# Optimization experiments

Measured on AMD Instinct MI355X. Metric: run time of the kernel, lower is better.

## Reference

```python
import jax, jax.numpy as jnp
import numpy as np

# Mamba-2 dims (from wrapper: d_model=hidden_size=2048, d_state=64, d_conv=4, expand=2, headdim=64)
D_MODEL = 2048
EXPAND = 2
HEADDIM = 64
D_STATE = 64
D_CONV = 4
D_INNER = EXPAND * D_MODEL            # 4096
NHEADS = D_INNER // HEADDIM           # 64
NGROUPS = 1                           # mamba_ssm default
CONV_DIM = D_INNER + 2 * NGROUPS * D_STATE          # 4224
D_IN_PROJ = 2 * D_INNER + 2 * NGROUPS * D_STATE + NHEADS  # 8384
BATCH = 1
SEQLEN = 1024
RMS_EPS = 1e-5


def setup_inputs() -> dict:
    key = jax.random.key(0)
    ks = jax.random.split(key, 8)
    x = jax.random.normal(ks[0], (BATCH, SEQLEN, D_MODEL), jnp.float32)
    W_in = jax.random.normal(ks[1], (D_IN_PROJ, D_MODEL), jnp.float32) * 0.02
    conv_w = jax.random.normal(ks[2], (CONV_DIM, D_CONV), jnp.float32) * 0.2
    conv_b = jnp.zeros((CONV_DIM,), jnp.float32)
    # dt_bias so that softplus(dt_raw + dt_bias) lands in a realistic dt range ~[1e-3, 5e-2]
    dt_bias = jax.random.uniform(ks[3], (NHEADS,), jnp.float32, -6.0, -3.0)
    # A = -exp(A_log), A_log init like mamba_ssm: A ~ Uniform(1, 16)
    A_log = jnp.log(1.0 + 15.0 * jax.random.uniform(ks[4], (NHEADS,), jnp.float32))
    D = jnp.ones((NHEADS,), jnp.float32)
    norm_w = jnp.ones((D_INNER,), jnp.float32)
    W_out = jax.random.normal(ks[5], (D_MODEL, D_INNER), jnp.float32) * 0.02
    return {"x": x, "W_in": W_in, "conv_w": conv_w, "conv_b": conv_b,
            "dt_bias": dt_bias, "A_log": A_log, "D": D, "norm_w": norm_w, "W_out": W_out}


def reference(x, W_in, conv_w, conv_b, dt_bias, A_log, D, norm_w, W_out):
    B, T, _ = x.shape
    # input projection -> [z | xBC | dt]
    zxbcdt = jnp.einsum('btd,pd->btp', x, W_in)
    z = zxbcdt[..., :D_INNER]                                  # [B,T,D_INNER] gate
    xBC = zxbcdt[..., D_INNER:D_INNER + CONV_DIM]              # [B,T,CONV_DIM]
    dt = jax.nn.softplus(zxbcdt[..., D_INNER + CONV_DIM:] + dt_bias)  # [B,T,H]
    # causal depthwise conv1d (kernel D_CONV) + SiLU
    xp = jnp.pad(xBC, ((0, 0), (D_CONV - 1, 0), (0, 0)))
    conv = conv_b + sum(xp[:, k:k + T, :] * conv_w[:, k] for k in range(D_CONV))
    xBC = jax.nn.silu(conv)
    xh = xBC[..., :D_INNER].reshape(B, T, NHEADS, HEADDIM)     # [B,T,H,P]
    Bm = xBC[..., D_INNER:D_INNER + D_STATE]                   # [B,T,N] (ngroups=1)
    Cm = xBC[..., D_INNER + D_STATE:]                          # [B,T,N]
    A = -jnp.exp(A_log)                                        # [H], negative
    dA = jnp.exp(dt * A)                                       # [B,T,H] decay per step

    def step(h, inp):
        # h: [B,H,P,N]
        dA_t, dt_t, B_t, x_t, C_t = inp
        h = h * dA_t[:, :, None, None] + jnp.einsum('bh,bn,bhp->bhpn', dt_t, B_t, x_t)
        y_t = jnp.einsum('bhpn,bn->bhp', h, C_t)
        return h, y_t

    h0 = jnp.zeros((B, NHEADS, HEADDIM, D_STATE), x.dtype)
    xs = (dA.transpose(1, 0, 2), dt.transpose(1, 0, 2), Bm.transpose(1, 0, 2),
          xh.transpose(1, 0, 2, 3), Cm.transpose(1, 0, 2))
    _, ys = jax.lax.scan(step, h0, xs)                         # ys: [T,B,H,P]
    y = ys.transpose(1, 0, 2, 3) + D[None, None, :, None] * xh  # skip term D*x
    y = y.reshape(B, T, D_INNER)
    # gated RMSNorm (norm_before_gate=False): norm(y * silu(z)) * weight
    y = y * jax.nn.silu(z)
    y = y * jax.lax.rsqrt(jnp.mean(y * y, axis=-1, keepdims=True) + RMS_EPS) * norm_w
    return jnp.einsum('bti,di->btd', y, W_out)
```

## Files before the change

kernel.cpp:

```cpp
#include <hip/hip_runtime.h>
#include <hip/hip_bf16.h>
#include <stdint.h>

#define SEQLEN   1024
#define DMODEL   2048
#define DINNER   4096
#define NHEADS   64
#define HEADDIM  64
#define DSTATE   64
#define CONVDIM  4224
#define DINPROJ  8384
#define RMS_EPS  1e-5f
#define CPAD     68
#define LP       72

typedef __attribute__((ext_vector_type(8))) __bf16 bf16x8;
typedef __attribute__((ext_vector_type(8))) unsigned short us8;
typedef __attribute__((ext_vector_type(4))) float f32x4;

__device__ __forceinline__ ushort f2bf(float f) {
    uint32_t u = __float_as_uint(f);
    u += 0x7FFFu + ((u >> 16) & 1u);
    return (ushort)(u >> 16);
}

__device__ __forceinline__ float bf2f(ushort u) {
    return __uint_as_float((uint32_t)u << 16);
}

__device__ __forceinline__ float silu(float a) { return a / (1.f + __expf(-a)); }

__device__ __forceinline__ void gload_lds16(const void* g, void* l) {
    __builtin_amdgcn_global_load_lds(
        (const __attribute__((address_space(1))) void*)g,
        (__attribute__((address_space(3))) void*)l, 16, 0, 0);
}

__global__ __launch_bounds__(256) void cvt3_kernel(
    const float* __restrict__ a, ushort* __restrict__ oa, int na4,
    const float* __restrict__ b, ushort* __restrict__ ob, int nb4,
    const float* __restrict__ c, ushort* __restrict__ oc, int nc4)
{
    int i = blockIdx.x * 256 + threadIdx.x;
    const float* src; ushort* dst;
    if (i < na4) { src = a; dst = oa; }
    else if (i < na4 + nb4) { i -= na4; src = b; dst = ob; }
    else { i -= na4 + nb4; if (i >= nc4) return; src = c; dst = oc; }
    float4 v = ((const float4*)src)[i];
    ushort4 o;
    o.x = f2bf(v.x); o.y = f2bf(v.y); o.z = f2bf(v.z); o.w = f2bf(v.w);
    ((ushort4*)dst)[i] = o;
}

__global__ __launch_bounds__(256, 4) void gemm4_bf16_nt(
    const __bf16* __restrict__ A, const __bf16* __restrict__ B,
    float* __restrict__ C, int M, int N, int K,
    int ntx, int nty, int nk, int ksteps, int swz)
{
    __shared__ __align__(16) __bf16 As[2][128 * 32];
    __shared__ __align__(16) __bf16 Bs[2][128 * 32];
    const int tid  = threadIdx.x;
    const int lane = tid & 63;
    const int wave = tid >> 6;
    const int wr = wave >> 1, wc = wave & 1;
    int id = blockIdx.x;
    if (swz) { int q = (ntx * nty * nk) >> 3; id = (id & 7) * q + (id >> 3); }
    const int kz  = id / (ntx * nty);
    const int rem = id % (ntx * nty);
    const int tx = rem / nty, ty = rem % nty;
    const int row0 = ty * 128, col0 = tx * 128;
    const int lr = lane & 15, lq = lane >> 4;
    const int rA = lane >> 2, jl = lane & 3;
    const int k0 = kz * ksteps * 32;

    const __bf16* srcA[2];
    const __bf16* srcB[2];
    int dstAB[2];
    #pragma unroll
    for (int e = 0; e < 2; ++e) {
        int r0 = (wave * 2 + e) * 16;
        int r  = r0 + rA;
        int jg = jl ^ ((rA >> 1) & 3);
        srcA[e] = A + (size_t)(row0 + r) * K + k0 + jg * 8;
        int gb = col0 + r; if (gb > N - 1) gb = N - 1;
        srcB[e] = B + (size_t)gb * K + k0 + jg * 8;
        dstAB[e] = r0 * 32;
    }

    f32x4 acc[4][4] = {};
    const int nt = ksteps;

#define STAGE(BUF)                                                            \
    _Pragma("unroll")                                                         \
    for (int e = 0; e < 2; ++e) {                                             \
        gload_lds16(srcA[e], &As[BUF][dstAB[e]]);                             \
        gload_lds16(srcB[e], &Bs[BUF][dstAB[e]]);                             \
        srcA[e] += 32; srcB[e] += 32;                                         \
    }

#define COMPUTE(BUF)                                                          \
    {                                                                         \
        bf16x8 af[4], bfr[4];                                                 \
        const int sl = (lq ^ ((lr >> 1) & 3)) * 8;                            \
        _Pragma("unroll")                                                     \
        for (int m = 0; m < 4; ++m) {                                         \
            int r = wr * 64 + m * 16 + lr;                                    \
            af[m] = *(const bf16x8*)(&As[BUF][r * 32 + sl]);                  \
        }                                                                     \
        _Pragma("unroll")                                                     \
        for (int n = 0; n < 4; ++n) {                                         \
            int r = wc * 64 + n * 16 + lr;                                    \
            bfr[n] = *(const bf16x8*)(&Bs[BUF][r * 32 + sl]);                 \
        }                                                                     \
        __builtin_amdgcn_s_setprio(1);                                        \
        _Pragma("unroll")                                                     \
        for (int m = 0; m < 4; ++m)                                           \
            _Pragma("unroll")                                                 \
            for (int n = 0; n < 4; ++n)                                       \
                acc[m][n] = __builtin_amdgcn_mfma_f32_16x16x32_bf16(af[m], bfr[n], acc[m][n], 0, 0, 0); \
        __builtin_amdgcn_s_setprio(0);                                        \
    }

    STAGE(0);
    asm volatile("s_waitcnt vmcnt(0)" ::: "memory");
    __builtin_amdgcn_s_barrier();
    asm volatile("" ::: "memory");

    for (int t = 0; t < nt; t += 2) {
        STAGE(1);
        COMPUTE(0);
        asm volatile("s_waitcnt vmcnt(0)" ::: "memory");
        __builtin_amdgcn_s_barrier();
        asm volatile("" ::: "memory");
        if (t + 2 < nt) { STAGE(0); }
        COMPUTE(1);
        asm volatile("s_waitcnt vmcnt(0)" ::: "memory");
        __builtin_amdgcn_s_barrier();
        asm volatile("" ::: "memory");
    }
#undef STAGE
#undef COMPUTE

    float* Co = C + (size_t)kz * M * N;
    #pragma unroll
    for (int m = 0; m < 4; ++m)
        #pragma unroll
        for (int n = 0; n < 4; ++n) {
            int col = col0 + wc * 64 + n * 16 + lr;
            if (col < N) {
                #pragma unroll
                for (int j = 0; j < 4; ++j) {
                    int row = row0 + wr * 64 + m * 16 + lq * 4 + j;
                    Co[(size_t)row * N + col] = acc[m][n][j];
                }
            }
        }
}

__global__ __launch_bounds__(256) void reduce4_scale_kernel(
    const float* __restrict__ p, const float* __restrict__ ssbuf,
    float* __restrict__ out, int n4)
{
    int i = blockIdx.x * 256 + threadIdx.x;
    if (i < n4) {
        int t = i >> 9;
        float sc = rsqrtf(ssbuf[t] * (1.f / DINNER) + RMS_EPS);
        float4 a = ((const float4*)p)[i];
        float4 b = ((const float4*)p)[i + n4];
        float4 c = ((const float4*)p)[i + 2 * (size_t)n4];
        float4 d = ((const float4*)p)[i + 3 * (size_t)n4];
        float4 o = {(a.x + b.x + c.x + d.x) * sc, (a.y + b.y + c.y + d.y) * sc,
                    (a.z + b.z + c.z + d.z) * sc, (a.w + b.w + c.w + d.w) * sc};
        ((float4*)out)[i] = o;
    }
}

__global__ __launch_bounds__(256, 3) void chunk_intra_kernel(
    const float* __restrict__ zx, const float* __restrict__ conv_w,
    const float* __restrict__ conv_b, const float* __restrict__ dt_bias,
    const float* __restrict__ A_log,
    float* __restrict__ x_scan, float* __restrict__ Cb,
    float* __restrict__ yintra, float* __restrict__ Tc, float* __restrict__ Ssum)
{
    const int head  = blockIdx.x >> 4;
    const int chunk = blockIdx.x & 15;
    const int t0 = chunk * 64;
    const int tid = threadIdx.x;
    const int lane = tid & 63, wv = tid >> 6;
    const int lr = lane & 15, lq = lane >> 4;

    __shared__ __align__(16) ushort XT [64 * LP];
    __shared__ __align__(16) ushort Crm[64 * LP];
    __shared__ __align__(16) ushort Brm[64 * LP];
    __shared__ __align__(16) ushort BnT[64 * LP];
    __shared__ __align__(16) ushort Grm[64 * LP];
    __shared__ float Sc[64], dts[64], ws[64];

    {
        const int p = lane;
        const int c = head * 64 + p;
        const float w0 = conv_w[c*4+0], w1 = conv_w[c*4+1];
        const float w2 = conv_w[c*4+2], w3 = conv_w[c*4+3];
        const float bia = conv_b[c];
        const int gt0 = t0 + wv * 16;
        const float* zc = zx + DINNER + c;
        float xm3 = (gt0 >= 3) ? zc[(size_t)(gt0-3)*DINPROJ] : 0.f;
        float xm2 = (gt0 >= 2) ? zc[(size_t)(gt0-2)*DINPROJ] : 0.f;
        float xm1 = (gt0 >= 1) ? zc[(size_t)(gt0-1)*DINPROJ] : 0.f;
        uint32_t pk[8];
        #pragma unroll
        for (int e = 0; e < 16; ++e) {
            float xt = zc[(size_t)(gt0+e)*DINPROJ];
            float s  = silu(bia + xm3*w0 + xm2*w1 + xm1*w2 + xt*w3);
            x_scan[(size_t)(gt0+e)*DINNER + c] = s;
            ushort b = f2bf(s);
            if (e & 1) pk[e>>1] |= (uint32_t)b << 16; else pk[e>>1] = (uint32_t)b;
            xm3 = xm2; xm2 = xm1; xm1 = xt;
        }
        int4 lo = { (int)pk[0], (int)pk[1], (int)pk[2], (int)pk[3] };
        int4 hi = { (int)pk[4], (int)pk[5], (int)pk[6], (int)pk[7] };
        *(int4*)&XT[p * LP + wv*16]     = lo;
        *(int4*)&XT[p * LP + wv*16 + 8] = hi;
    }

    #pragma unroll
    for (int k = 0; k < 4; ++k) {
        int n0 = wv * 16 + k * 4;
        int gt = t0 + lane;
        {
            float4 w0 = *(const float4*)&conv_w[(4096 + n0 + 0) * 4];
            float4 w1 = *(const float4*)&conv_w[(4096 + n0 + 1) * 4];
            float4 w2 = *(const float4*)&conv_w[(4096 + n0 + 2) * 4];
            float4 w3 = *(const float4*)&conv_w[(4096 + n0 + 3) * 4];
            float4 bv = *(const float4*)&conv_b[4096 + n0];
            float4 r0 = {0,0,0,0}, r1 = {0,0,0,0}, r2 = {0,0,0,0}, r3;
            const float* base = zx + (size_t)gt * DINPROJ + 8192 + n0;
            if (gt >= 3) r0 = *(const float4*)(base - 3 * DINPROJ);
            if (gt >= 2) r1 = *(const float4*)(base - 2 * DINPROJ);
            if (gt >= 1) r2 = *(const float4*)(base - 1 * DINPROJ);
            r3 = *(const float4*)base;
            ushort b0 = f2bf(silu(bv.x + r0.x*w0.x + r1.x*w0.y + r2.x*w0.z + r3.x*w0.w));
            ushort b1 = f2bf(silu(bv.y + r0.y*w1.x + r1.y*w1.y + r2.y*w1.z + r3.y*w1.w));
            ushort b2 = f2bf(silu(bv.z + r0.z*w2.x + r1.z*w2.y + r2.z*w2.z + r3.z*w2.w));
            ushort b3 = f2bf(silu(bv.w + r0.w*w3.x + r1.w*w3.y + r2.w*w3.z + r3.w*w3.w));
            uint2 pk = { (uint32_t)b0 | ((uint32_t)b1 << 16),
                         (uint32_t)b2 | ((uint32_t)b3 << 16) };
            *(uint2*)&Brm[lane * LP + n0] = pk;
            BnT[(n0+0)*LP + lane] = b0; BnT[(n0+1)*LP + lane] = b1;
            BnT[(n0+2)*LP + lane] = b2; BnT[(n0+3)*LP + lane] = b3;
        }
        {
            float4 w0 = *(const float4*)&conv_w[(4160 + n0 + 0) * 4];
            float4 w1 = *(const float4*)&conv_w[(4160 + n0 + 1) * 4];
            float4 w2 = *(const float4*)&conv_w[(4160 + n0 + 2) * 4];
            float4 w3 = *(const float4*)&conv_w[(4160 + n0 + 3) * 4];
            float4 bv = *(const float4*)&conv_b[4160 + n0];
            float4 r0 = {0,0,0,0}, r1 = {0,0,0,0}, r2 = {0,0,0,0}, r3;
            const float* base = zx + (size_t)gt * DINPROJ + 8256 + n0;
            if (gt >= 3) r0 = *(const float4*)(base - 3 * DINPROJ);
            if (gt >= 2) r1 = *(const float4*)(base - 2 * DINPROJ);
            if (gt >= 1) r2 = *(const float4*)(base - 1 * DINPROJ);
            r3 = *(const float4*)base;
            float4 cv;
            cv.x = silu(bv.x + r0.x*w0.x + r1.x*w0.y + r2.x*w0.z + r3.x*w0.w);
            cv.y = silu(bv.y + r0.y*w1.x + r1.y*w1.y + r2.y*w1.z + r3.y*w1.w);
            cv.z = silu(bv.z + r0.z*w2.x + r1.z*w2.y + r2.z*w2.z + r3.z*w2.w);
            cv.w = silu(bv.w + r0.w*w3.x + r1.w*w3.y + r2.w*w3.z + r3.w*w3.w);
            uint2 pk = { (uint32_t)f2bf(cv.x) | ((uint32_t)f2bf(cv.y) << 16),
                         (uint32_t)f2bf(cv.z) | ((uint32_t)f2bf(cv.w) << 16) };
            *(uint2*)&Crm[lane * LP + n0] = pk;
            if (head == 0) *(float4*)&Cb[(size_t)gt * 64 + n0] = cv;
        }
    }

    if (wv == 1) {
        float raw = zx[(size_t)(t0 + lane) * DINPROJ + 8320 + head] + dt_bias[head];
        float dt  = (raw > 20.f) ? raw : log1pf(__expf(raw));
        dts[lane] = dt;
        float v = dt * (-__expf(A_log[head]));
        #pragma unroll
        for (int off = 1; off < 64; off <<= 1) {
            float u = __shfl_up(v, off, 64);
            if (lane >= off) v += u;
        }
        Sc[lane] = v;
        Ssum[(t0 + lane) * 64 + head] = v;
    }
    __syncthreads();
    if (tid < 64) ws[tid] = dts[tid] * __expf(Sc[63] - Sc[tid]);

    const int i0 = wv * 16;
    f32x4 gf[4] = {};
    #pragma unroll
    for (int kk = 0; kk < 2; ++kk) {
        bf16x8 a = __builtin_bit_cast(bf16x8,
            *(const us8*)&Crm[(i0 + lr) * LP + lq*8 + kk*32]);
        #pragma unroll
        for (int f = 0; f < 4; ++f) {
            bf16x8 b = __builtin_bit_cast(bf16x8,
                *(const us8*)&Brm[(f*16 + lr) * LP + lq*8 + kk*32]);
            gf[f] = __builtin_amdgcn_mfma_f32_16x16x32_bf16(a, b, gf[f], 0, 0, 0);
        }
    }
    {
        float Si[4];
        #pragma unroll
        for (int j = 0; j < 4; ++j) Si[j] = Sc[i0 + lq*4 + j];
        #pragma unroll
        for (int f = 0; f < 4; ++f) {
            int s = f*16 + lr;
            float dw = dts[s], Ss_ = Sc[s];
            #pragma unroll
            for (int j = 0; j < 4; ++j) {
                int i = i0 + lq*4 + j;
                float v = (s <= i) ? gf[f][j] * dw * __expf(Si[j] - Ss_) : 0.f;
                Grm[i * LP + s] = f2bf(v);
            }
        }
    }
    __syncthreads();

    const int p0 = i0;
    bf16x8 xa[2], xw[2];
    #pragma unroll
    for (int kk = 0; kk < 2; ++kk) {
        us8 raw = *(const us8*)&XT[(p0 + lr) * LP + lq*8 + kk*32];
        xa[kk] = __builtin_bit_cast(bf16x8, raw);
        us8 sw;
        #pragma unroll
        for (int e = 0; e < 8; ++e) {
            int s = lq*8 + kk*32 + e;
            sw[e] = f2bf(bf2f(raw[e]) * ws[s]);
        }
        xw[kk] = __builtin_bit_cast(bf16x8, sw);
    }
    f32x4 yf[4] = {};
    f32x4 tf[4] = {};
    #pragma unroll
    for (int kk = 0; kk < 2; ++kk) {
        #pragma unroll
        for (int f = 0; f < 4; ++f) {
            bf16x8 gb = __builtin_bit_cast(bf16x8,
                *(const us8*)&Grm[(f*16 + lr) * LP + lq*8 + kk*32]);
            yf[f] = __builtin_amdgcn_mfma_f32_16x16x32_bf16(xa[kk], gb, yf[f], 0, 0, 0);
            bf16x8 bb = __builtin_bit_cast(bf16x8,
                *(const us8*)&BnT[(f*16 + lr) * LP + lq*8 + kk*32]);
            tf[f] = __builtin_amdgcn_mfma_f32_16x16x32_bf16(xw[kk], bb, tf[f], 0, 0, 0);
        }
    }
    float* tcb = Tc + (size_t)(head * 16 + chunk) * 4096;
    #pragma unroll
    for (int f = 0; f < 4; ++f) {
        int col = f*16 + lr;
        int p   = p0 + lq*4;
        float4 yv = {yf[f][0], yf[f][1], yf[f][2], yf[f][3]};
        *(float4*)&yintra[(size_t)(t0 + col) * DINNER + head*64 + p] = yv;
        #pragma unroll
        for (int j = 0; j < 4; ++j)
            tcb[(p + j) * 64 + col] = tf[f][j];
    }
}

__global__ __launch_bounds__(256) void chunk_state_kernel(
    float* __restrict__ Tc, const float* __restrict__ Ssum)
{
    const int head = blockIdx.x;
    const int tid = threadIdx.x;
    float h[16] = {};
    float* base = Tc + (size_t)head * 16 * 4096 + tid * 16;
    for (int c = 0; c < 16; ++c) {
        float Q = __expf(Ssum[(c * 64 + 63) * 64 + head]);
        float4* p = (float4*)(base + (size_t)c * 4096);
        #pragma unroll
        for (int v = 0; v < 4; ++v) {
            float4 t = p[v];
            float4 hold = {h[v*4], h[v*4+1], h[v*4+2], h[v*4+3]};
            h[v*4+0] = h[v*4+0] * Q + t.x;
            h[v*4+1] = h[v*4+1] * Q + t.y;
            h[v*4+2] = h[v*4+2] * Q + t.z;
            h[v*4+3] = h[v*4+3] * Q + t.w;
            p[v] = hold;
        }
    }
}

__global__ __launch_bounds__(256) void inter_combine_kernel(
    const float* __restrict__ Hpre, const float* __restrict__ Cb,
    const float* __restrict__ Ssum, const float* __restrict__ yintra,
    const float* __restrict__ x_scan, const float* __restrict__ zx,
    const float* __restrict__ Dv, const float* __restrict__ norm_w,
    ushort* __restrict__ ybf, float* __restrict__ ssbuf)
{
    const int head  = blockIdx.x >> 4;
    const int chunk = blockIdx.x & 15;
    const int t0 = chunk * 64;
    const int tid = threadIdx.x;
    const int ty = tid >> 4, tx = tid & 15;
    const int lane = tid & 63, wv = tid >> 6;

    __shared__ __align__(16) float HsT[64][CPAD];
    __shared__ __align__(16) float CsT[64][CPAD];
    __shared__ float Se[64];

    const float* hb = Hpre + (size_t)(head * 16 + chunk) * 4096;
    #pragma unroll
    for (int k = 0; k < 4; ++k) {
        int n0 = wv * 16 + k * 4;
        float4 h = *(const float4*)&hb[lane * 64 + n0];
        float4 c = *(const float4*)&Cb[(t0 + lane) * 64 + n0];
        HsT[n0][lane] = h.x; HsT[n0+1][lane] = h.y; HsT[n0+2][lane] = h.z; HsT[n0+3][lane] = h.w;
        CsT[n0][lane] = c.x; CsT[n0+1][lane] = c.y; CsT[n0+2][lane] = c.z; CsT[n0+3][lane] = c.w;
    }
    if (tid < 64) Se[tid] = __expf(Ssum[(t0 + tid) * 64 + head]);
    __syncthreads();

    float acc[4][4] = {};
    for (int n = 0; n < 64; ++n) {
        float4 ci = *(const float4*)&CsT[n][ty * 4];
        float4 hp = *(const float4*)&HsT[n][tx * 4];
        acc[0][0] += ci.x*hp.x; acc[0][1] += ci.x*hp.y; acc[0][2] += ci.x*hp.z; acc[0][3] += ci.x*hp.w;
        acc[1][0] += ci.y*hp.x; acc[1][1] += ci.y*hp.y; acc[1][2] += ci.y*hp.z; acc[1][3] += ci.y*hp.w;
        acc[2][0] += ci.z*hp.x; acc[2][1] += ci.z*hp.y; acc[2][2] += ci.z*hp.z; acc[2][3] += ci.z*hp.w;
        acc[3][0] += ci.w*hp.x; acc[3][1] += ci.w*hp.y; acc[3][2] += ci.w*hp.z; acc[3][3] += ci.w*hp.w;
    }

    const float Dh = Dv[head];
    const int col = head * 64 + tx * 4;
    float4 nw = *(const float4*)&norm_w[col];
    float ssp[4];
    #pragma unroll
    for (int di = 0; di < 4; ++di) {
        int t = t0 + ty * 4 + di;
        float se = Se[ty * 4 + di];
        float4 yi = *(const float4*)&yintra[(size_t)t * DINNER + col];
        float4 xh = *(const float4*)&x_scan[(size_t)t * DINNER + col];
        float4 zv = *(const float4*)&zx[(size_t)t * DINPROJ + col];
        float4 y;
        y.x = (acc[di][0] * se + yi.x + Dh * xh.x) * silu(zv.x);
        y.y = (acc[di][1] * se + yi.y + Dh * xh.y) * silu(zv.y);
        y.z = (acc[di][2] * se + yi.z + Dh * xh.z) * silu(zv.z);
        y.w = (acc[di][3] * se + yi.w + Dh * xh.w) * silu(zv.w);
        ssp[di] = y.x*y.x + y.y*y.y + y.z*y.z + y.w*y.w;
        ushort4 o;
        o.x = f2bf(y.x * nw.x); o.y = f2bf(y.y * nw.y);
        o.z = f2bf(y.z * nw.z); o.w = f2bf(y.w * nw.w);
        *(ushort4*)&ybf[(size_t)t * DINNER + col] = o;
    }
    #pragma unroll
    for (int di = 0; di < 4; ++di) {
        float s = ssp[di];
        s += __shfl_xor(s, 1, 64);
        s += __shfl_xor(s, 2, 64);
        s += __shfl_xor(s, 4, 64);
        s += __shfl_xor(s, 8, 64);
        if (tx == 0) atomicAdd(&ssbuf[t0 + ty * 4 + di], s);
    }
}

extern "C" void kernel_launch(void* const* d_in, const int* in_sizes, int n_in,
                              void* d_out, int out_size, void* d_ws, size_t ws_size,
                              hipStream_t stream)
{
    const float* x       = (const float*)d_in[0];
    const float* W_in    = (const float*)d_in[1];
    const float* conv_w  = (const float*)d_in[2];
    const float* conv_b  = (const float*)d_in[3];
    const float* dt_bias = (const float*)d_in[4];
    const float* A_log   = (const float*)d_in[5];
    const float* Dv      = (const float*)d_in[6];
    const float* norm_w  = (const float*)d_in[7];
    const float* W_out   = (const float*)d_in[8];
    float* out = (float*)d_out;

    char* ws = (char*)d_ws;
    const size_t OFF_WIN  = 0;
    const size_t OFF_WOUT = 34340864;
    const size_t OFF_XBF  = OFF_WOUT + 16777216;
    const size_t OFF_ZX   = OFF_XBF + 4194304;
    const size_t OFF_XSC  = OFF_ZX + 34340864;
    const size_t OFF_CB   = OFF_XSC + 16777216;
    const size_t OFF_SSB  = OFF_CB + 262144;
    const size_t OFF_YBF  = OFF_SSB + 4096;
    const size_t OFF_TC   = OFF_YBF + 8388608;
    const size_t OFF_SS   = OFF_TC + 16777216;

    ushort* WinBf  = (ushort*)(ws + OFF_WIN);
    ushort* WoutBf = (ushort*)(ws + OFF_WOUT);
    ushort* xBf    = (ushort*)(ws + OFF_XBF);
    float*  zxb    = (float*)(ws + OFF_ZX);
    float*  xsc    = (float*)(ws + OFF_XSC);
    float*  Cb     = (float*)(ws + OFF_CB);
    float*  ssbuf  = (float*)(ws + OFF_SSB);
    ushort* ybf    = (ushort*)(ws + OFF_YBF);
    float*  Tc     = (float*)(ws + OFF_TC);
    float*  Ssum   = (float*)(ws + OFF_SS);
    float*  yintra = (float*)(ws + OFF_WIN);
    float*  part   = (float*)(ws + OFF_WIN);

    const int nW4 = DINPROJ * DMODEL / 4;
    const int nO4 = DMODEL * DINNER / 4;
    const int nX4 = SEQLEN * DMODEL / 4;
    const int nAll = nW4 + nO4 + nX4;
    cvt3_kernel<<<(nAll + 255) / 256, 256, 0, stream>>>(
        W_in, WinBf, nW4, W_out, WoutBf, nO4, x, xBf, nX4);

    hipMemsetAsync(ssbuf, 0, SEQLEN * sizeof(float), stream);

    gemm4_bf16_nt<<<528, 256, 0, stream>>>(
        (const __bf16*)xBf, (const __bf16*)WinBf, zxb,
        SEQLEN, DINPROJ, DMODEL, 66, 8, 1, DMODEL / 32, 1);

    chunk_intra_kernel<<<1024, 256, 0, stream>>>(
        zxb, conv_w, conv_b, dt_bias, A_log, xsc, Cb, yintra, Tc, Ssum);

    chunk_state_kernel<<<64, 256, 0, stream>>>(Tc, Ssum);

    inter_combine_kernel<<<1024, 256, 0, stream>>>(
        Tc, Cb, Ssum, yintra, xsc, zxb, Dv, norm_w, ybf, ssbuf);

    gemm4_bf16_nt<<<512, 256, 0, stream>>>(
        (const __bf16*)ybf, (const __bf16*)WoutBf, part,
        SEQLEN, DMODEL, DINNER, 16, 8, 4, DINNER / 32 / 4, 1);

    reduce4_scale_kernel<<<(SEQLEN * DMODEL / 4 + 255) / 256, 256, 0, stream>>>(
        part, ssbuf, out, SEQLEN * DMODEL / 4);
}
```

Before: 185.2 us.

## Fuse weight fp32-to-bf16 conversion into GEMM B-tile loading

Removes the separate pre-pass that converted W_in and W_out to bf16. The GEMM now loads fp32 B tiles into registers, converts them to bf16, and writes them to LDS with the same swizzle, while the A operand still uses direct global-to-LDS loads. This avoids writing and re-reading about 50 MB of bf16 weights per call. In exchange, B-tile reads double in bytes, each tile is re-read once per row tile, and the writes now go through registers with an extra lgkmcnt wait before each barrier.

```diff
diff --git a/kernel.cpp b/kernel.cpp
--- a/kernel.cpp
+++ b/kernel.cpp
@@ -36,24 +36,19 @@
         (__attribute__((address_space(3))) void*)l, 16, 0, 0);
 }
 
-__global__ __launch_bounds__(256) void cvt3_kernel(
-    const float* __restrict__ a, ushort* __restrict__ oa, int na4,
-    const float* __restrict__ b, ushort* __restrict__ ob, int nb4,
-    const float* __restrict__ c, ushort* __restrict__ oc, int nc4)
-{
+__global__ __launch_bounds__(256) void cvt1_kernel(const float* __restrict__ in,
+                                                   ushort* __restrict__ out, int n4) {
     int i = blockIdx.x * 256 + threadIdx.x;
-    const float* src; ushort* dst;
-    if (i < na4) { src = a; dst = oa; }
-    else if (i < na4 + nb4) { i -= na4; src = b; dst = ob; }
-    else { i -= na4 + nb4; if (i >= nc4) return; src = c; dst = oc; }
-    float4 v = ((const float4*)src)[i];
-    ushort4 o;
-    o.x = f2bf(v.x); o.y = f2bf(v.y); o.z = f2bf(v.z); o.w = f2bf(v.w);
-    ((ushort4*)dst)[i] = o;
+    if (i < n4) {
+        float4 v = ((const float4*)in)[i];
+        ushort4 o;
+        o.x = f2bf(v.x); o.y = f2bf(v.y); o.z = f2bf(v.z); o.w = f2bf(v.w);
+        ((ushort4*)out)[i] = o;
+    }
 }
 
 __global__ __launch_bounds__(256, 4) void gemm4_bf16_nt(
-    const __bf16* __restrict__ A, const __bf16* __restrict__ B,
+    const __bf16* __restrict__ A, const float* __restrict__ B,
     float* __restrict__ C, int M, int N, int K,
     int ntx, int nty, int nk, int ksteps, int swz)
 {
@@ -74,28 +69,50 @@
     const int k0 = kz * ksteps * 32;
 
     const __bf16* srcA[2];
-    const __bf16* srcB[2];
-    int dstAB[2];
+    int dstA[2];
     #pragma unroll
     for (int e = 0; e < 2; ++e) {
         int r0 = (wave * 2 + e) * 16;
         int r  = r0 + rA;
         int jg = jl ^ ((rA >> 1) & 3);
         srcA[e] = A + (size_t)(row0 + r) * K + k0 + jg * 8;
+        dstA[e] = r0 * 32;
+    }
+    const float* srcBf[4];
+    int dstB[4];
+    #pragma unroll
+    for (int p = 0; p < 4; ++p) {
+        int r = p * 32 + (tid >> 3);
+        int j = tid & 7;
         int gb = col0 + r; if (gb > N - 1) gb = N - 1;
-        srcB[e] = B + (size_t)gb * K + k0 + jg * 8;
-        dstAB[e] = r0 * 32;
-    }
+        srcBf[p] = B + (size_t)gb * K + k0 + j * 4;
+        int sp = (j >> 1) ^ ((r >> 1) & 3);
+        dstB[p] = r * 32 + sp * 8 + (j & 1) * 4;
+    }
+    float4 bregs[4];
 
     f32x4 acc[4][4] = {};
     const int nt = ksteps;
 
-#define STAGE(BUF)                                                            \
+#define STAGE_LOAD(BUF)                                                       \
     _Pragma("unroll")                                                         \
     for (int e = 0; e < 2; ++e) {                                             \
-        gload_lds16(srcA[e], &As[BUF][dstAB[e]]);                             \
-        gload_lds16(srcB[e], &Bs[BUF][dstAB[e]]);                             \
-        srcA[e] += 32; srcB[e] += 32;                                         \
+        gload_lds16(srcA[e], &As[BUF][dstA[e]]);                              \
+        srcA[e] += 32;                                                        \
+    }                                                                         \
+    _Pragma("unroll")                                                         \
+    for (int p = 0; p < 4; ++p) {                                             \
+        bregs[p] = *(const float4*)srcBf[p];                                  \
+        srcBf[p] += 32;                                                       \
+    }
+
+#define STAGE_WRITE(BUF)                                                      \
+    _Pragma("unroll")                                                         \
+    for (int p = 0; p < 4; ++p) {                                             \
+        __bf16 h0 = (__bf16)bregs[p].x, h1 = (__bf16)bregs[p].y;              \
+        __bf16 h2 = (__bf16)bregs[p].z, h3 = (__bf16)bregs[p].w;              \
+        __bf16* d = &Bs[BUF][dstB[p]];                                        \
+        d[0] = h0; d[1] = h1; d[2] = h2; d[3] = h3;                           \
     }
 
 #define COMPUTE(BUF)                                                          \
@@ -121,24 +138,31 @@
         __builtin_amdgcn_s_setprio(0);                                        \
     }
 
-    STAGE(0);
+    STAGE_LOAD(0);
     asm volatile("s_waitcnt vmcnt(0)" ::: "memory");
+    STAGE_WRITE(0);
+    asm volatile("s_waitcnt lgkmcnt(0)" ::: "memory");
     __builtin_amdgcn_s_barrier();
     asm volatile("" ::: "memory");
 
     for (int t = 0; t < nt; t += 2) {
-        STAGE(1);
+        STAGE_LOAD(1);
         COMPUTE(0);
         asm volatile("s_waitcnt vmcnt(0)" ::: "memory");
+        STAGE_WRITE(1);
+        asm volatile("s_waitcnt lgkmcnt(0)" ::: "memory");
         __builtin_amdgcn_s_barrier();
         asm volatile("" ::: "memory");
-        if (t + 2 < nt) { STAGE(0); }
+        if (t + 2 < nt) { STAGE_LOAD(0); }
         COMPUTE(1);
         asm volatile("s_waitcnt vmcnt(0)" ::: "memory");
+        if (t + 2 < nt) { STAGE_WRITE(0); }
+        asm volatile("s_waitcnt lgkmcnt(0)" ::: "memory");
         __builtin_amdgcn_s_barrier();
         asm volatile("" ::: "memory");
     }
-#undef STAGE
+#undef STAGE_LOAD
+#undef STAGE_WRITE
 #undef COMPUTE
 
     float* Co = C + (size_t)kz * M * N;
@@ -484,8 +508,6 @@
     const size_t OFF_TC   = OFF_YBF + 8388608;
     const size_t OFF_SS   = OFF_TC + 16777216;
 
-    ushort* WinBf  = (ushort*)(ws + OFF_WIN);
-    ushort* WoutBf = (ushort*)(ws + OFF_WOUT);
     ushort* xBf    = (ushort*)(ws + OFF_XBF);
     float*  zxb    = (float*)(ws + OFF_ZX);
     float*  xsc    = (float*)(ws + OFF_XSC);
@@ -497,17 +519,13 @@
     float*  yintra = (float*)(ws + OFF_WIN);
     float*  part   = (float*)(ws + OFF_WIN);
 
-    const int nW4 = DINPROJ * DMODEL / 4;
-    const int nO4 = DMODEL * DINNER / 4;
     const int nX4 = SEQLEN * DMODEL / 4;
-    const int nAll = nW4 + nO4 + nX4;
-    cvt3_kernel<<<(nAll + 255) / 256, 256, 0, stream>>>(
-        W_in, WinBf, nW4, W_out, WoutBf, nO4, x, xBf, nX4);
+    cvt1_kernel<<<(nX4 + 255) / 256, 256, 0, stream>>>(x, xBf, nX4);
 
     hipMemsetAsync(ssbuf, 0, SEQLEN * sizeof(float), stream);
 
     gemm4_bf16_nt<<<528, 256, 0, stream>>>(
-        (const __bf16*)xBf, (const __bf16*)WinBf, zxb,
+        (const __bf16*)xBf, W_in, zxb,
         SEQLEN, DINPROJ, DMODEL, 66, 8, 1, DMODEL / 32, 1);
 
     chunk_intra_kernel<<<1024, 256, 0, stream>>>(
@@ -519,7 +537,7 @@
         Tc, Cb, Ssum, yintra, xsc, zxb, Dv, norm_w, ybf, ssbuf);
 
     gemm4_bf16_nt<<<512, 256, 0, stream>>>(
-        (const __bf16*)ybf, (const __bf16*)WoutBf, part,
+        (const __bf16*)ybf, W_out, part,
         SEQLEN, DMODEL, DINNER, 16, 8, 4, DINNER / 32 / 4, 1);
 
     reduce4_scale_kernel<<<(SEQLEN * DMODEL / 4 + 255) / 256, 256, 0, stream>>>(
```

Result: slower. 347.2 us (+87.5%).
